# Optimization experiments

Measured on AMD Instinct MI355X. Metric: run time of the kernel, lower is better.

The kernel has to match this reference:

```python
import jax, jax.numpy as jnp
import numpy as np

N, D, H, E, TOP_K = 4096, 1024, 4096, 8, 2


def setup_inputs() -> dict:
    key = jax.random.key(0)
    ks = jax.random.split(key, 12)
    s_in = 1.0 / np.sqrt(D)
    s_hid = 1.0 / np.sqrt(H)
    return {
        "x": jax.random.normal(ks[0], (N, D), dtype=jnp.float32),
        "gate_w": jax.random.uniform(ks[1], (D, E), jnp.float32, -s_in, s_in),
        "gate_b": jax.random.uniform(ks[2], (E,), jnp.float32, -s_in, s_in),
        "w1": jax.random.uniform(ks[3], (E, D, H), jnp.float32, -s_in, s_in),
        "b1": jax.random.uniform(ks[4], (E, H), jnp.float32, -s_in, s_in),
        "w2": jax.random.uniform(ks[5], (E, H, D), jnp.float32, -s_hid, s_hid),
        "b2": jax.random.uniform(ks[6], (E, D), jnp.float32, -s_hid, s_hid),
        "sw1": jax.random.uniform(ks[7], (D, H), jnp.float32, -s_in, s_in),
        "sb1": jax.random.uniform(ks[8], (H,), jnp.float32, -s_in, s_in),
        "sw2": jax.random.uniform(ks[9], (H, D), jnp.float32, -s_hid, s_hid),
        "sb2": jax.random.uniform(ks[10], (D,), jnp.float32, -s_hid, s_hid),
    }


def reference(x, gate_w, gate_b, w1, b1, w2, b2, sw1, sb1, sw2, sb2):
    # Gating
    gate_logits = x @ gate_w + gate_b                      # [N, E]
    gate_probs = jax.nn.softmax(gate_logits, axis=-1)      # [N, E]
    top_logits, selected = jax.lax.top_k(gate_logits, TOP_K)  # [N, K]
    top_w = jax.nn.softmax(top_logits, axis=-1).astype(x.dtype)
    # Dense combine weights: [N, E], zero for unselected experts
    combine = (jax.nn.one_hot(selected, E, dtype=x.dtype) * top_w[..., None]).sum(axis=1)
    # All-expert FFN (exact GELU like torch nn.GELU default)
    h = jax.nn.gelu(jnp.einsum('nd,edh->enh', x, w1) + b1[:, None, :], approximate=False)
    y = jnp.einsum('enh,ehd->end', h, w2) + b2[:, None, :]  # [E, N, D]
    results = jnp.einsum('end,ne->nd', y, combine)
    # Shared expert
    sh = jax.nn.gelu(x @ sw1 + sb1, approximate=False)
    results = results + sh @ sw2 + sb2
    # Aux load-balancing loss
    importance = gate_probs.sum(axis=0)                     # [E]
    load = jax.nn.one_hot(selected, E, dtype=jnp.float32).sum(axis=(0, 1))
    importance = importance / (importance.sum() + 1e-8)
    load = load / (load.sum() + 1e-8)
    aux_loss = jnp.sum((importance - load) ** 2)
    return results, aux_loss
```

## Files before the change

kernel.cpp:

```cpp
#include <hip/hip_runtime.h>
#include <hip/hip_bf16.h>

#define N_TOK 4096
#define DIM   1024
#define HID   4096
#define NE    8
#define ROW_CAP128 13312
#define ROW_CAP64  12800

typedef unsigned short ushort_t;
typedef short bf16x8 __attribute__((ext_vector_type(8)));
typedef float f32x4 __attribute__((ext_vector_type(4)));

__device__ __forceinline__ ushort_t f2bf(float f) {
    unsigned int u = __float_as_uint(f);
    u += 0x7fffu + ((u >> 16) & 1u);
    return (ushort_t)(u >> 16);
}
__device__ __forceinline__ float bf2f(ushort_t u) {
    return __uint_as_float(((unsigned int)u) << 16);
}
__device__ __forceinline__ float gelu_f(float v) {
    return 0.5f * v * (1.0f + erff(v * 0.70710678118654752f));
}
__device__ __forceinline__ void async_load16(const void* g, void* l) {
    __builtin_amdgcn_global_load_lds(
        (const __attribute__((address_space(1))) void*)g,
        (__attribute__((address_space(3))) void*)l, 16, 0, 0);
}
__device__ __forceinline__ void fma4x4(const float4& a, const float4& b, float acc[4][4]) {
    acc[0][0] = fmaf(a.x, b.x, acc[0][0]); acc[0][1] = fmaf(a.x, b.y, acc[0][1]);
    acc[0][2] = fmaf(a.x, b.z, acc[0][2]); acc[0][3] = fmaf(a.x, b.w, acc[0][3]);
    acc[1][0] = fmaf(a.y, b.x, acc[1][0]); acc[1][1] = fmaf(a.y, b.y, acc[1][1]);
    acc[1][2] = fmaf(a.y, b.z, acc[1][2]); acc[1][3] = fmaf(a.y, b.w, acc[1][3]);
    acc[2][0] = fmaf(a.z, b.x, acc[2][0]); acc[2][1] = fmaf(a.z, b.y, acc[2][1]);
    acc[2][2] = fmaf(a.z, b.z, acc[2][2]); acc[2][3] = fmaf(a.z, b.w, acc[2][3]);
    acc[3][0] = fmaf(a.w, b.x, acc[3][0]); acc[3][1] = fmaf(a.w, b.y, acc[3][1]);
    acc[3][2] = fmaf(a.w, b.z, acc[3][2]); acc[3][3] = fmaf(a.w, b.w, acc[3][3]);
}

__global__ __launch_bounds__(256) void gate_kernel(
    const float* __restrict__ x, const float* __restrict__ gw, const float* __restrict__ gb,
    int* __restrict__ counts, float* __restrict__ importance,
    int* __restrict__ sel, float* __restrict__ selw)
{
    __shared__ float s_imp[NE];
    __shared__ int   s_cnt[NE];
    int tid = threadIdx.x;
    if (tid < NE) { s_imp[tid] = 0.f; s_cnt[tid] = 0; }
    __syncthreads();

    int wave = tid >> 6, lane = tid & 63;
    int n = blockIdx.x * 4 + wave;

    float acc[NE];
#pragma unroll
    for (int e = 0; e < NE; ++e) acc[e] = 0.f;

    const float* xr = x + (size_t)n * DIM;
    for (int it = 0; it < DIM / 64; ++it) {
        int d = it * 64 + lane;
        float xv = xr[d];
        const float4* g = (const float4*)(gw + (size_t)d * NE);
        float4 g0 = g[0], g1 = g[1];
        acc[0] = fmaf(xv, g0.x, acc[0]); acc[1] = fmaf(xv, g0.y, acc[1]);
        acc[2] = fmaf(xv, g0.z, acc[2]); acc[3] = fmaf(xv, g0.w, acc[3]);
        acc[4] = fmaf(xv, g1.x, acc[4]); acc[5] = fmaf(xv, g1.y, acc[5]);
        acc[6] = fmaf(xv, g1.z, acc[6]); acc[7] = fmaf(xv, g1.w, acc[7]);
    }
#pragma unroll
    for (int off = 32; off > 0; off >>= 1) {
#pragma unroll
        for (int e = 0; e < NE; ++e) acc[e] += __shfl_down(acc[e], off, 64);
    }

    if (lane == 0) {
        float lg[NE], p[NE];
        float mx = -1e30f;
#pragma unroll
        for (int e = 0; e < NE; ++e) { lg[e] = acc[e] + gb[e]; mx = fmaxf(mx, lg[e]); }
        float se = 0.f;
#pragma unroll
        for (int e = 0; e < NE; ++e) { p[e] = expf(lg[e] - mx); se += p[e]; }
        float inv = 1.f / se;
#pragma unroll
        for (int e = 0; e < NE; ++e) atomicAdd(&s_imp[e], p[e] * inv);
        int i1 = 0;
#pragma unroll
        for (int e = 1; e < NE; ++e) if (lg[e] > lg[i1]) i1 = e;
        int i2 = -1;
#pragma unroll
        for (int e = 0; e < NE; ++e) if (e != i1 && (i2 < 0 || lg[e] > lg[i2])) i2 = e;
        float t = expf(lg[i2] - lg[i1]);
        float wA = 1.f / (1.f + t), wB = t / (1.f + t);
        sel[n * 2] = i1; sel[n * 2 + 1] = i2;
        selw[n * 2] = wA; selw[n * 2 + 1] = wB;
        atomicAdd(&s_cnt[i1], 1); atomicAdd(&s_cnt[i2], 1);
    }
    __syncthreads();
    if (tid < NE) {
        atomicAdd(&importance[tid], s_imp[tid]);
        atomicAdd(&counts[tid], s_cnt[tid]);
    }
}

__global__ void plan_kernel(
    const int* __restrict__ counts, const float* __restrict__ importance,
    int* __restrict__ cursors, int* __restrict__ offs, int* __restrict__ total_rows,
    int* __restrict__ row_token, float* __restrict__ row_wt, float* __restrict__ out_aux,
    int al)
{
    __shared__ int s_offs[NE + 1], s_cnt[NE];
    if (threadIdx.x == 0) {
        int o = 0;
        for (int e = 0; e < NE; ++e) {
            s_cnt[e] = counts[e];
            s_offs[e] = o;
            cursors[e] = o;
            o += (s_cnt[e] + al - 1) & ~(al - 1);
        }
        s_offs[NE] = o;
        for (int e = 0; e <= NE; ++e) offs[e] = s_offs[e];
        *total_rows = o + N_TOK;
        float is = 1e-8f, ls = 1e-8f;
        for (int e = 0; e < NE; ++e) { is += importance[e]; ls += (float)s_cnt[e]; }
        float aux = 0.f;
        for (int e = 0; e < NE; ++e) {
            float d = importance[e] / is - (float)s_cnt[e] / ls;
            aux += d * d;
        }
        *out_aux = aux;
    }
    __syncthreads();
    for (int e = 0; e < NE; ++e) {
        int st = s_offs[e] + s_cnt[e], en = s_offs[e + 1];
        for (int i = st + (int)threadIdx.x; i < en; i += (int)blockDim.x) {
            row_token[i] = -1; row_wt[i] = 0.f;
        }
    }
}

__global__ __launch_bounds__(256) void scatter_kernel(
    const int* __restrict__ sel, const float* __restrict__ selw,
    int* __restrict__ cursors, const int* __restrict__ offs,
    int* __restrict__ row_token, float* __restrict__ row_wt)
{
    int n = blockIdx.x * 256 + threadIdx.x;
#pragma unroll
    for (int k = 0; k < 2; ++k) {
        int e = sel[n * 2 + k];
        int pos = atomicAdd(&cursors[e], 1);
        row_token[pos] = n;
        row_wt[pos] = selw[n * 2 + k];
    }
    int off8 = offs[NE];
    row_token[off8 + n] = n;
    row_wt[off8 + n] = 1.0f;
}

__global__ __launch_bounds__(256) void cvt_x_kernel(
    const float* __restrict__ x, ushort_t* __restrict__ xb)
{
    int i = (blockIdx.x * 256 + threadIdx.x) * 8;
    float4 a = *(const float4*)(x + i);
    float4 b = *(const float4*)(x + i + 4);
    uint4 o;
    o.x = ((unsigned)f2bf(a.y) << 16) | f2bf(a.x);
    o.y = ((unsigned)f2bf(a.w) << 16) | f2bf(a.z);
    o.z = ((unsigned)f2bf(b.y) << 16) | f2bf(b.x);
    o.w = ((unsigned)f2bf(b.w) << 16) | f2bf(b.z);
    *(uint4*)(xb + i) = o;
}

__global__ __launch_bounds__(256) void transpose_bf16(
    const float* __restrict__ src, ushort_t* __restrict__ dst, int K, int N)
{
    __shared__ ushort_t T[64][80];
    size_t eoff = (size_t)blockIdx.z * K * N;
    src += eoff; dst += eoff;
    int n0 = blockIdx.x * 64, k0 = blockIdx.y * 64;
    int t = threadIdx.x;
    int cq = (t & 15) * 4;
    int kr = t >> 4;
#pragma unroll
    for (int rI = 0; rI < 4; ++rI) {
        int k = kr + rI * 16;
        float4 v = *(const float4*)(src + (size_t)(k0 + k) * N + n0 + cq);
        T[cq + 0][k] = f2bf(v.x);
        T[cq + 1][k] = f2bf(v.y);
        T[cq + 2][k] = f2bf(v.z);
        T[cq + 3][k] = f2bf(v.w);
    }
    __syncthreads();
    int nr = t >> 2;
    int kq = (t & 3) * 16;
    uint4 o0 = *(const uint4*)&T[nr][kq];
    uint4 o1 = *(const uint4*)&T[nr][kq + 8];
    ushort_t* dp = dst + (size_t)(n0 + nr) * K + k0 + kq;
    *(uint4*)dp = o0;
    *(uint4*)(dp + 8) = o1;
}

__global__ __launch_bounds__(256) void ffn1_mfma(
    const ushort_t* __restrict__ xb, const ushort_t* __restrict__ wtbuf,
    const float* __restrict__ b1, const float* __restrict__ sb1,
    const int* __restrict__ offs, const int* __restrict__ total_rows,
    const int* __restrict__ row_token, ushort_t* __restrict__ hbuf)
{
    const int row0 = blockIdx.x * 128;
    if (row0 >= *total_rows) return;
    const int col0 = blockIdx.y * 128;

    int e = 0;
#pragma unroll
    for (int i = 0; i < NE; ++i) e += (row0 >= offs[i + 1]) ? 1 : 0;
    const ushort_t* W = wtbuf + (size_t)e * (HID * DIM);
    const float* Bv = (e < NE) ? (b1 + (size_t)e * HID) : sb1;

    __shared__ ushort_t As[4096];
    __shared__ ushort_t Bs[4096];

    const int tid = threadIdx.x;
    const int lane = tid & 63;
    const int w = tid >> 6;
    const int wm = w & 1, wn = w >> 1;
    const int lm = lane & 15, lk = lane >> 4;

    const int sS = 2 * w;
    int r0 = row0 + (sS + 0) * 16 + lm;
    int r1 = row0 + (sS + 1) * 16 + lm;
    int t0 = row_token[r0]; if (t0 < 0) t0 = 0;
    int t1 = row_token[r1]; if (t1 < 0) t1 = 0;
    const ushort_t* gA0 = xb + (size_t)t0 * DIM + lk * 8;
    const ushort_t* gA1 = xb + (size_t)t1 * DIM + lk * 8;
    const ushort_t* gB0 = W + (size_t)(col0 + (sS + 0) * 16 + lm) * DIM + lk * 8;
    const ushort_t* gB1 = W + (size_t)(col0 + (sS + 1) * 16 + lm) * DIM + lk * 8;
    ushort_t* lA0 = &As[(sS + 0) * 512];
    ushort_t* lA1 = &As[(sS + 1) * 512];
    ushort_t* lB0 = &Bs[(sS + 0) * 512];
    ushort_t* lB1 = &Bs[(sS + 1) * 512];

    f32x4 zero = {0.f, 0.f, 0.f, 0.f};
    f32x4 acc[4][4];
#pragma unroll
    for (int i = 0; i < 4; ++i)
#pragma unroll
        for (int j = 0; j < 4; ++j) acc[i][j] = zero;

    const bf16x8* Af = (const bf16x8*)As;
    const bf16x8* Bf = (const bf16x8*)Bs;

    for (int k0 = 0; k0 < DIM; k0 += 32) {
        async_load16(gA0 + k0, lA0);
        async_load16(gA1 + k0, lA1);
        async_load16(gB0 + k0, lB0);
        async_load16(gB1 + k0, lB1);
        __syncthreads();
        bf16x8 a[4], b[4];
#pragma unroll
        for (int i = 0; i < 4; ++i) a[i] = Af[(wm * 4 + i) * 64 + lane];
#pragma unroll
        for (int j = 0; j < 4; ++j) b[j] = Bf[(wn * 4 + j) * 64 + lane];
#pragma unroll
        for (int i = 0; i < 4; ++i)
#pragma unroll
            for (int j = 0; j < 4; ++j)
                acc[i][j] = __builtin_amdgcn_mfma_f32_16x16x32_bf16(a[i], b[j], acc[i][j], 0, 0, 0);
        __syncthreads();
    }

#pragma unroll
    for (int j = 0; j < 4; ++j) {
        int C = col0 + (wn * 4 + j) * 16 + lm;
        float bj = Bv[C];
#pragma unroll
        for (int i = 0; i < 4; ++i) {
            int Rb = row0 + (wm * 4 + i) * 16 + lk * 4;
#pragma unroll
            for (int r = 0; r < 4; ++r) {
                float v = gelu_f(acc[i][j][r] + bj);
                hbuf[(size_t)(Rb + r) * HID + C] = f2bf(v);
            }
        }
    }
}

__global__ __launch_bounds__(256) void ffn2_mfma(
    const ushort_t* __restrict__ hbuf, const ushort_t* __restrict__ wtbuf,
    const float* __restrict__ b2, const float* __restrict__ sb2,
    const int* __restrict__ offs, const int* __restrict__ total_rows,
    const int* __restrict__ row_token, const float* __restrict__ row_wt,
    float* __restrict__ out)
{
    const int row0 = blockIdx.x * 128;
    if (row0 >= *total_rows) return;
    const int col0 = blockIdx.y * 128;

    int e = 0;
#pragma unroll
    for (int i = 0; i < NE; ++i) e += (row0 >= offs[i + 1]) ? 1 : 0;
    const ushort_t* W = wtbuf + (size_t)e * (HID * DIM);
    const float* Bv = (e < NE) ? (b2 + (size_t)e * DIM) : sb2;

    __shared__ ushort_t As[4096];
    __shared__ ushort_t Bs[4096];
    __shared__ int   s_tok[128];
    __shared__ float s_wt[128];

    const int tid = threadIdx.x;
    if (tid < 128) { s_tok[tid] = row_token[row0 + tid]; s_wt[tid] = row_wt[row0 + tid]; }

    const int lane = tid & 63;
    const int w = tid >> 6;
    const int wm = w & 1, wn = w >> 1;
    const int lm = lane & 15, lk = lane >> 4;

    const int sS = 2 * w;
    const ushort_t* gA0 = hbuf + (size_t)(row0 + (sS + 0) * 16 + lm) * HID + lk * 8;
    const ushort_t* gA1 = hbuf + (size_t)(row0 + (sS + 1) * 16 + lm) * HID + lk * 8;
    const ushort_t* gB0 = W + (size_t)(col0 + (sS + 0) * 16 + lm) * HID + lk * 8;
    const ushort_t* gB1 = W + (size_t)(col0 + (sS + 1) * 16 + lm) * HID + lk * 8;
    ushort_t* lA0 = &As[(sS + 0) * 512];
    ushort_t* lA1 = &As[(sS + 1) * 512];
    ushort_t* lB0 = &Bs[(sS + 0) * 512];
    ushort_t* lB1 = &Bs[(sS + 1) * 512];

    f32x4 zero = {0.f, 0.f, 0.f, 0.f};
    f32x4 acc[4][4];
#pragma unroll
    for (int i = 0; i < 4; ++i)
#pragma unroll
        for (int j = 0; j < 4; ++j) acc[i][j] = zero;

    const bf16x8* Af = (const bf16x8*)As;
    const bf16x8* Bf = (const bf16x8*)Bs;

    for (int k0 = 0; k0 < HID; k0 += 32) {
        async_load16(gA0 + k0, lA0);
        async_load16(gA1 + k0, lA1);
        async_load16(gB0 + k0, lB0);
        async_load16(gB1 + k0, lB1);
        __syncthreads();
        bf16x8 a[4], b[4];
#pragma unroll
        for (int i = 0; i < 4; ++i) a[i] = Af[(wm * 4 + i) * 64 + lane];
#pragma unroll
        for (int j = 0; j < 4; ++j) b[j] = Bf[(wn * 4 + j) * 64 + lane];
#pragma unroll
        for (int i = 0; i < 4; ++i)
#pragma unroll
            for (int j = 0; j < 4; ++j)
                acc[i][j] = __builtin_amdgcn_mfma_f32_16x16x32_bf16(a[i], b[j], acc[i][j], 0, 0, 0);
        __syncthreads();
    }

#pragma unroll
    for (int j = 0; j < 4; ++j) {
        int C = col0 + (wn * 4 + j) * 16 + lm;
        float bj = Bv[C];
#pragma unroll
        for (int i = 0; i < 4; ++i) {
            int rb = (wm * 4 + i) * 16 + lk * 4;
#pragma unroll
            for (int r = 0; r < 4; ++r) {
                int tok = s_tok[rb + r];
                if (tok < 0) continue;
                float v = s_wt[rb + r] * (acc[i][j][r] + bj);
                atomicAdd(&out[(size_t)tok * DIM + C], v);
            }
        }
    }
}

__global__ __launch_bounds__(256) void ffn1_kernel(
    const float* __restrict__ x, const float* __restrict__ w1, const float* __restrict__ b1,
    const float* __restrict__ sw1, const float* __restrict__ sb1,
    const int* __restrict__ offs, const int* __restrict__ total_rows,
    const int* __restrict__ row_token, ushort_t* __restrict__ hbuf)
{
    int row0 = blockIdx.x * 64;
    if (row0 >= *total_rows) return;
    int col0 = blockIdx.y * 64;
    int e = 0;
#pragma unroll
    for (int i = 1; i <= NE; ++i) if (row0 >= offs[i]) e = i;
    const float* W = (e < NE) ? w1 + (size_t)e * DIM * HID : sw1;
    const float* B = (e < NE) ? b1 + (size_t)e * HID : sb1;

    __shared__ float As_[16][68];
    __shared__ float Bs_[16][64];
    __shared__ int toks[64];
    int tid = threadIdx.x;
    if (tid < 64) toks[tid] = row_token[row0 + tid];
    __syncthreads();

    int am = tid >> 2, ak = (tid & 3) << 2;
    int bkr = tid >> 4, bn = (tid & 15) << 2;
    int tx = tid & 15, ty = tid >> 4;
    int tok = toks[am];
    const float* ap = x + (size_t)(tok >= 0 ? tok : 0) * DIM + ak;
    const float* bp = W + (size_t)bkr * HID + col0 + bn;

    float acc[4][4] = {};
    for (int k0 = 0; k0 < DIM; k0 += 16) {
        float4 av = make_float4(0.f, 0.f, 0.f, 0.f);
        if (tok >= 0) av = *(const float4*)(ap + k0);
        float4 bv = *(const float4*)(bp + (size_t)k0 * HID);
        As_[ak + 0][am] = av.x; As_[ak + 1][am] = av.y;
        As_[ak + 2][am] = av.z; As_[ak + 3][am] = av.w;
        *(float4*)&Bs_[bkr][bn] = bv;
        __syncthreads();
#pragma unroll
        for (int kk = 0; kk < 16; ++kk) {
            float4 a = *(const float4*)&As_[kk][ty * 4];
            float4 b = *(const float4*)&Bs_[kk][tx * 4];
            fma4x4(a, b, acc);
        }
        __syncthreads();
    }
    float4 bb = *(const float4*)(B + col0 + tx * 4);
    ushort_t* hp = hbuf + (size_t)(row0 + ty * 4) * HID + col0 + tx * 4;
#pragma unroll
    for (int r = 0; r < 4; ++r) {
        ushort4 pk;
        pk.x = f2bf(gelu_f(acc[r][0] + bb.x));
        pk.y = f2bf(gelu_f(acc[r][1] + bb.y));
        pk.z = f2bf(gelu_f(acc[r][2] + bb.z));
        pk.w = f2bf(gelu_f(acc[r][3] + bb.w));
        *(ushort4*)(hp + (size_t)r * HID) = pk;
    }
}

__global__ __launch_bounds__(256) void ffn2_kernel(
    const ushort_t* __restrict__ hbuf,
    const float* __restrict__ w2, const float* __restrict__ b2,
    const float* __restrict__ sw2, const float* __restrict__ sb2,
    const int* __restrict__ offs, const int* __restrict__ total_rows,
    const int* __restrict__ row_token, const float* __restrict__ row_wt,
    float* __restrict__ out)
{
    int row0 = blockIdx.x * 64;
    if (row0 >= *total_rows) return;
    int col0 = blockIdx.y * 64;
    int e = 0;
#pragma unroll
    for (int i = 1; i <= NE; ++i) if (row0 >= offs[i]) e = i;
    const float* W = (e < NE) ? w2 + (size_t)e * HID * DIM : sw2;
    const float* B = (e < NE) ? b2 + (size_t)e * DIM : sb2;

    __shared__ float As_[16][68];
    __shared__ float Bs_[16][64];
    __shared__ int toks[64];
    __shared__ float wts[64];
    int tid = threadIdx.x;
    if (tid < 64) { toks[tid] = row_token[row0 + tid]; wts[tid] = row_wt[row0 + tid]; }
    __syncthreads();

    int am = tid >> 2, ak = (tid & 3) << 2;
    int bkr = tid >> 4, bn = (tid & 15) << 2;
    int tx = tid & 15, ty = tid >> 4;
    const ushort_t* ap = hbuf + (size_t)(row0 + am) * HID + ak;
    const float* bp = W + (size_t)bkr * DIM + col0 + bn;

    float acc[4][4] = {};
    for (int k0 = 0; k0 < HID; k0 += 16) {
        ushort4 hv = *(const ushort4*)(ap + k0);
        float4 bv = *(const float4*)(bp + (size_t)k0 * DIM);
        As_[ak + 0][am] = bf2f(hv.x); As_[ak + 1][am] = bf2f(hv.y);
        As_[ak + 2][am] = bf2f(hv.z); As_[ak + 3][am] = bf2f(hv.w);
        *(float4*)&Bs_[bkr][bn] = bv;
        __syncthreads();
#pragma unroll
        for (int kk = 0; kk < 16; ++kk) {
            float4 a = *(const float4*)&As_[kk][ty * 4];
            float4 b = *(const float4*)&Bs_[kk][tx * 4];
            fma4x4(a, b, acc);
        }
        __syncthreads();
    }
    float4 bb = *(const float4*)(B + col0 + tx * 4);
#pragma unroll
    for (int r = 0; r < 4; ++r) {
        int rr = ty * 4 + r;
        int tok = toks[rr];
        if (tok < 0) continue;
        float w = wts[rr];
        float* op = out + (size_t)tok * DIM + col0 + tx * 4;
        atomicAdd(&op[0], w * (acc[r][0] + bb.x));
        atomicAdd(&op[1], w * (acc[r][1] + bb.y));
        atomicAdd(&op[2], w * (acc[r][2] + bb.z));
        atomicAdd(&op[3], w * (acc[r][3] + bb.w));
    }
}

extern "C" void kernel_launch(void* const* d_in, const int* in_sizes, int n_in,
                              void* d_out, int out_size, void* d_ws, size_t ws_size,
                              hipStream_t stream)
{
    const float* x   = (const float*)d_in[0];
    const float* gw  = (const float*)d_in[1];
    const float* gb  = (const float*)d_in[2];
    const float* w1  = (const float*)d_in[3];
    const float* b1  = (const float*)d_in[4];
    const float* w2  = (const float*)d_in[5];
    const float* b2  = (const float*)d_in[6];
    const float* sw1 = (const float*)d_in[7];
    const float* sb1 = (const float*)d_in[8];
    const float* sw2 = (const float*)d_in[9];
    const float* sb2 = (const float*)d_in[10];
    float* out = (float*)d_out;

    char* ws = (char*)d_ws;
    int*   counts     = (int*)(ws + 0);
    int*   cursors    = (int*)(ws + 32);
    int*   offs       = (int*)(ws + 64);
    int*   total_rows = (int*)(ws + 100);
    float* importance = (float*)(ws + 128);
    int*   sel        = (int*)(ws + 256);
    float* selw       = (float*)(ws + 33024);
    int*   row_token  = (int*)(ws + 65792);
    float* row_wt     = (float*)(ws + 119040);

    const size_t XB_OFF = 262144;
    const size_t WT_OFF = XB_OFF + (size_t)N_TOK * DIM * 2;
    const size_t HB_OFF = WT_OFF + (size_t)9 * HID * DIM * 2;
    const size_t NEED   = HB_OFF + (size_t)ROW_CAP128 * HID * 2;
    ushort_t* xb    = (ushort_t*)(ws + XB_OFF);
    ushort_t* wtbuf = (ushort_t*)(ws + WT_OFF);
    const size_t DH = (size_t)HID * DIM;

    hipMemsetAsync(d_out, 0, (size_t)out_size * sizeof(float), stream);
    hipMemsetAsync(d_ws, 0, 256, stream);

    gate_kernel<<<N_TOK / 4, 256, 0, stream>>>(x, gw, gb, counts, importance, sel, selw);

    if (ws_size >= NEED) {
        ushort_t* hbuf = (ushort_t*)(ws + HB_OFF);
        plan_kernel<<<1, 64, 0, stream>>>(counts, importance, cursors, offs, total_rows,
                                          row_token, row_wt, out + (size_t)N_TOK * DIM, 128);
        scatter_kernel<<<N_TOK / 256, 256, 0, stream>>>(sel, selw, cursors, offs, row_token, row_wt);
        cvt_x_kernel<<<(N_TOK * DIM) / 2048, 256, 0, stream>>>(x, xb);
        transpose_bf16<<<dim3(HID / 64, DIM / 64, NE), 256, 0, stream>>>(w1, wtbuf, DIM, HID);
        transpose_bf16<<<dim3(HID / 64, DIM / 64, 1), 256, 0, stream>>>(sw1, wtbuf + 8 * DH, DIM, HID);
        ffn1_mfma<<<dim3(ROW_CAP128 / 128, HID / 128), 256, 0, stream>>>(
            xb, wtbuf, b1, sb1, offs, total_rows, row_token, hbuf);
        transpose_bf16<<<dim3(DIM / 64, HID / 64, NE), 256, 0, stream>>>(w2, wtbuf, HID, DIM);
        transpose_bf16<<<dim3(DIM / 64, HID / 64, 1), 256, 0, stream>>>(sw2, wtbuf + 8 * DH, HID, DIM);
        ffn2_mfma<<<dim3(ROW_CAP128 / 128, DIM / 128), 256, 0, stream>>>(
            hbuf, wtbuf, b2, sb2, offs, total_rows, row_token, row_wt, out);
    } else {
        ushort_t* hbuf = (ushort_t*)(ws + 262144);
        plan_kernel<<<1, 64, 0, stream>>>(counts, importance, cursors, offs, total_rows,
                                          row_token, row_wt, out + (size_t)N_TOK * DIM, 64);
        scatter_kernel<<<N_TOK / 256, 256, 0, stream>>>(sel, selw, cursors, offs, row_token, row_wt);
        ffn1_kernel<<<dim3(ROW_CAP64 / 64, HID / 64), 256, 0, stream>>>(
            x, w1, b1, sw1, sb1, offs, total_rows, row_token, hbuf);
        ffn2_kernel<<<dim3(ROW_CAP64 / 64, DIM / 64), 256, 0, stream>>>(
            hbuf, w2, b2, sw2, sb2, offs, total_rows, row_token, row_wt, out);
    }
}
```

Before: 1.000 ms.

## Split-K the second FFN GEMM, swap grid axes, merge shared-expert transposes

```diff
diff --git a/kernel.cpp b/kernel.cpp
--- a/kernel.cpp
+++ b/kernel.cpp
@@ -173,11 +173,12 @@
 }
 
 __global__ __launch_bounds__(256) void transpose_bf16(
-    const float* __restrict__ src, ushort_t* __restrict__ dst, int K, int N)
+    const float* __restrict__ src, const float* __restrict__ srcS,
+    ushort_t* __restrict__ dst, int K, int N)
 {
     __shared__ ushort_t T[64][80];
-    size_t eoff = (size_t)blockIdx.z * K * N;
-    src += eoff; dst += eoff;
+    const float* s = (blockIdx.z < 8) ? (src + (size_t)blockIdx.z * K * N) : srcS;
+    dst += (size_t)blockIdx.z * K * N;
     int n0 = blockIdx.x * 64, k0 = blockIdx.y * 64;
     int t = threadIdx.x;
     int cq = (t & 15) * 4;
@@ -185,7 +186,7 @@
 #pragma unroll
     for (int rI = 0; rI < 4; ++rI) {
         int k = kr + rI * 16;
-        float4 v = *(const float4*)(src + (size_t)(k0 + k) * N + n0 + cq);
+        float4 v = *(const float4*)(s + (size_t)(k0 + k) * N + n0 + cq);
         T[cq + 0][k] = f2bf(v.x);
         T[cq + 1][k] = f2bf(v.y);
         T[cq + 2][k] = f2bf(v.z);
@@ -207,9 +208,9 @@
     const int* __restrict__ offs, const int* __restrict__ total_rows,
     const int* __restrict__ row_token, ushort_t* __restrict__ hbuf)
 {
-    const int row0 = blockIdx.x * 128;
+    const int row0 = blockIdx.y * 128;
     if (row0 >= *total_rows) return;
-    const int col0 = blockIdx.y * 128;
+    const int col0 = blockIdx.x * 128;
 
     int e = 0;
 #pragma unroll
@@ -292,9 +293,11 @@
     const int* __restrict__ row_token, const float* __restrict__ row_wt,
     float* __restrict__ out)
 {
-    const int row0 = blockIdx.x * 128;
+    const int row0 = blockIdx.y * 128;
     if (row0 >= *total_rows) return;
-    const int col0 = blockIdx.y * 128;
+    const int col0 = blockIdx.x * 128;
+    const int kc = blockIdx.z;
+    const int kLo = kc * (HID / 2), kHi = kLo + (HID / 2);
 
     int e = 0;
 #pragma unroll
@@ -335,7 +338,7 @@
     const bf16x8* Af = (const bf16x8*)As;
     const bf16x8* Bf = (const bf16x8*)Bs;
 
-    for (int k0 = 0; k0 < HID; k0 += 32) {
+    for (int k0 = kLo; k0 < kHi; k0 += 32) {
         async_load16(gA0 + k0, lA0);
         async_load16(gA1 + k0, lA1);
         async_load16(gB0 + k0, lB0);
@@ -357,7 +360,7 @@
 #pragma unroll
     for (int j = 0; j < 4; ++j) {
         int C = col0 + (wn * 4 + j) * 16 + lm;
-        float bj = Bv[C];
+        float bj = (kc == 0) ? Bv[C] : 0.f;
 #pragma unroll
         for (int i = 0; i < 4; ++i) {
             int rb = (wm * 4 + i) * 16 + lk * 4;
@@ -527,7 +530,6 @@
     const size_t NEED   = HB_OFF + (size_t)ROW_CAP128 * HID * 2;
     ushort_t* xb    = (ushort_t*)(ws + XB_OFF);
     ushort_t* wtbuf = (ushort_t*)(ws + WT_OFF);
-    const size_t DH = (size_t)HID * DIM;
 
     hipMemsetAsync(d_out, 0, (size_t)out_size * sizeof(float), stream);
     hipMemsetAsync(d_ws, 0, 256, stream);
@@ -540,13 +542,11 @@
                                           row_token, row_wt, out + (size_t)N_TOK * DIM, 128);
         scatter_kernel<<<N_TOK / 256, 256, 0, stream>>>(sel, selw, cursors, offs, row_token, row_wt);
         cvt_x_kernel<<<(N_TOK * DIM) / 2048, 256, 0, stream>>>(x, xb);
-        transpose_bf16<<<dim3(HID / 64, DIM / 64, NE), 256, 0, stream>>>(w1, wtbuf, DIM, HID);
-        transpose_bf16<<<dim3(HID / 64, DIM / 64, 1), 256, 0, stream>>>(sw1, wtbuf + 8 * DH, DIM, HID);
-        ffn1_mfma<<<dim3(ROW_CAP128 / 128, HID / 128), 256, 0, stream>>>(
+        transpose_bf16<<<dim3(HID / 64, DIM / 64, 9), 256, 0, stream>>>(w1, sw1, wtbuf, DIM, HID);
+        ffn1_mfma<<<dim3(HID / 128, ROW_CAP128 / 128), 256, 0, stream>>>(
             xb, wtbuf, b1, sb1, offs, total_rows, row_token, hbuf);
-        transpose_bf16<<<dim3(DIM / 64, HID / 64, NE), 256, 0, stream>>>(w2, wtbuf, HID, DIM);
-        transpose_bf16<<<dim3(DIM / 64, HID / 64, 1), 256, 0, stream>>>(sw2, wtbuf + 8 * DH, HID, DIM);
-        ffn2_mfma<<<dim3(ROW_CAP128 / 128, DIM / 128), 256, 0, stream>>>(
+        transpose_bf16<<<dim3(DIM / 64, HID / 64, 9), 256, 0, stream>>>(w2, sw2, wtbuf, HID, DIM);
+        ffn2_mfma<<<dim3(DIM / 128, ROW_CAP128 / 128, 2), 256, 0, stream>>>(
             hbuf, wtbuf, b2, sb2, offs, total_rows, row_token, row_wt, out);
     } else {
         ushort_t* hbuf = (ushort_t*)(ws + 262144);
```

After: 968.7 us. 1.03x faster.
